# Optimization experiments

Measured on AMD Instinct MI355X. Metric: run time of the kernel, lower is better.

## Reference

```python
import jax, jax.numpy as jnp
import numpy as np

B, T, F, S, H, A = 32768, 64, 64, 5, 128, 16  # batch, obs_len, fut_len, state, hidden, adapter


def _gru_cell(x, h, Wih, Whh, bih, bhh):
    # PyTorch GRUCell math: gates ordered (r, z, n)
    gx = x @ Wih.T + bih
    gh = h @ Whh.T + bhh
    rx, zx, nx = jnp.split(gx, 3, axis=-1)
    rh, zh, nh = jnp.split(gh, 3, axis=-1)
    r = jax.nn.sigmoid(rx + rh)
    z = jax.nn.sigmoid(zx + zh)
    n = jnp.tanh(nx + r * nh)
    return (1.0 - z) * n + z * h


def setup_inputs() -> dict:
    key = jax.random.key(0)
    ks = jax.random.split(key, 24)
    p = lambda k, shp: jax.random.normal(k, shp, jnp.float32) * 0.05
    return {
        "obs": jax.random.normal(ks[0], (B, T, S), jnp.float32),
        "target": jax.random.normal(ks[1], (B, F, S), jnp.float32),
        "dataset_ids": jax.random.randint(ks[2], (B,), 0, 4),
        "enc_Wih": p(ks[3], (3 * H, S)), "enc_Whh": p(ks[4], (3 * H, H)),
        "enc_bih": p(ks[5], (3 * H,)), "enc_bhh": p(ks[6], (3 * H,)),
        "cell_Wih": p(ks[7], (3 * H, S)), "cell_Whh": p(ks[8], (3 * H, H)),
        "cell_bih": p(ks[9], (3 * H,)), "cell_bhh": p(ks[10], (3 * H,)),
        "head_W": p(ks[11], (S, H)), "head_b": p(ks[12], (S,)),
        "pp_W1": p(ks[13], (A, H)), "pp_b1": p(ks[14], (A,)),
        "pp_W2": p(ks[15], (H, A)), "pp_b2": p(ks[16], (H,)),
        "pk_W1": p(ks[17], (A, H)), "pk_b1": p(ks[18], (A,)),
        "pk_W2": p(ks[19], (H, A)), "pk_b2": p(ks[20], (H,)),
    }


def reference(obs, target, dataset_ids,
              enc_Wih, enc_Whh, enc_bih, enc_bhh,
              cell_Wih, cell_Whh, cell_bih, cell_bhh,
              head_W, head_b,
              pp_W1, pp_b1, pp_W2, pp_b2,
              pk_W1, pk_b1, pk_W2, pk_b2):
    b = obs.shape[0]
    # Encoder GRU over obs -> final hidden state [B, H]
    h0 = jnp.zeros((b, H), obs.dtype)
    def enc_step(h, x):
        return _gru_cell(x, h, enc_Wih, enc_Whh, enc_bih, enc_bhh), None
    h_t, _ = jax.lax.scan(enc_step, h0, jnp.swapaxes(obs, 0, 1))

    pm = (dataset_ids == 0)[:, None]  # pointodyssey routed to private_point
    km = (dataset_ids == 1)[:, None]  # kubric routed to private_kubric

    def adapt(h):
        dp = jax.nn.relu(h @ pp_W1.T + pp_b1) @ pp_W2.T + pp_b2
        dk = jax.nn.relu(h @ pk_W1.T + pk_b1) @ pk_W2.T + pk_b2
        return h + jnp.where(pm, dp, 0.0) + jnp.where(km, dk, 0.0)

    # Teacher-forced inputs: x_0 = obs[:, -1], x_t = target[:, t-1]
    xs = jnp.concatenate([obs[:, -1:, :], target[:, :-1, :]], axis=1)  # [B, F, S]
    def roll_step(h, x):
        h = _gru_cell(x, h, cell_Wih, cell_Whh, cell_bih, cell_bhh)
        h = adapt(h)
        return h, h @ head_W.T + head_b
    _, preds = jax.lax.scan(roll_step, h_t, jnp.swapaxes(xs, 0, 1))  # [F, B, S]
    return jnp.swapaxes(preds, 0, 1)  # [B, F, S]
```

## Files before the change

kernel.cpp:

```cpp
#include <hip/hip_runtime.h>

#define B_TOT 32768
#define T_OBS 64
#define F_FUT 64
#define S_DIM 5
#define H_DIM 128
#define A_DIM 16
#define R_BLK 64
#define NTHREADS 512
#define XSTR 320
#define HSTR 128
#define XPAD 36
#define APAD 24

#define LOG2E 1.4426950408889634f
#define L2E2  2.8853900817779268f

typedef __attribute__((ext_vector_type(8))) short short8;
typedef __attribute__((ext_vector_type(4))) float f32x4;

union U8 { short8 v; unsigned int u[4]; unsigned short s[8]; };

#if __has_builtin(__builtin_amdgcn_exp2f)
#define EXP2(x) __builtin_amdgcn_exp2f(x)
#else
#define EXP2(x) exp2f(x)
#endif

__device__ __forceinline__ unsigned short f2bf(float f) {
  unsigned int u = __float_as_uint(f);
  u += 0x7FFFu + ((u >> 16) & 1u);
  return (unsigned short)(u >> 16);
}

__device__ __forceinline__ unsigned cvtpk(float a, float b) {
  unsigned r;
  asm("v_cvt_pk_bf16_f32 %0, %1, %2" : "=v"(r) : "v"(a), "v"(b));
  return r;
}

__device__ __forceinline__ f32x4 MFMA(short8 a, short8 b, f32x4 c) {
  return __builtin_amdgcn_mfma_f32_16x16x32_bf16(a, b, c, 0, 0, 0);
}

__device__ __forceinline__ short8 h_read(const unsigned short* base, int row, int ks, int lg) {
  return *(const short8*)(base + row * HSTR + (((4 * ks + lg + row) & 15) << 3));
}
__device__ __forceinline__ void h_write(unsigned short* base, int row, int w, int lg,
                                        unsigned lo, unsigned hi) {
  unsigned short* p = base + row * HSTR +
                      (((4 * (w >> 1) + lg + row) & 15) << 3) + ((w & 1) << 2);
  *(uint2*)p = make_uint2(lo, hi);
}

__device__ __forceinline__ short8 load_w(const float* __restrict__ W, int ld,
                                         int g0, int gmax, int kmax, int ks,
                                         int lr, int lg, float scale) {
  U8 a;
  const int g = g0 + lr;
  #pragma unroll
  for (int i = 0; i < 8; ++i) {
    int k = 32 * ks + 16 * (i >> 2) + 4 * lg + (i & 3);
    float v = (g < gmax && k < kmax) ? W[g * ld + k] * scale : 0.0f;
    a.s[i] = f2bf(v);
  }
  return a.v;
}

__device__ __forceinline__ void setup_weights(
    const float* __restrict__ Wih, const float* __restrict__ Whh,
    const float* __restrict__ bih, const float* __restrict__ bhh,
    short8 (&fh)[3][4], short8 (&fx)[3],
    f32x4& brz0, f32x4& brz1, f32x4& bnh, f32x4& bnx,
    int w, int lr, int lg)
{
  #pragma unroll
  for (int t = 0; t < 3; ++t) {
    const float sc = (t == 2) ? L2E2 : LOG2E;
    #pragma unroll
    for (int ks = 0; ks < 4; ++ks)
      fh[t][ks] = load_w(Whh, H_DIM, t * H_DIM + 16 * w, 384, H_DIM, ks, lr, lg, sc);
    fx[t] = load_w(Wih, S_DIM, t * H_DIM + 16 * w, 384, S_DIM, 0, lr, lg, sc);
  }
  #pragma unroll
  for (int i = 0; i < 4; ++i) {
    int g = 16 * w + 4 * lg + i;
    brz0[i] = (bih[g] + bhh[g]) * LOG2E;
    brz1[i] = (bih[H_DIM + g] + bhh[H_DIM + g]) * LOG2E;
    bnh[i]  = bhh[2 * H_DIM + g] * L2E2;
    bnx[i]  = bih[2 * H_DIM + g] * L2E2;
  }
}

__device__ __forceinline__ void mfma_rt(
    const unsigned short* __restrict__ hb, const unsigned short* __restrict__ xb,
    int row, int lg,
    const short8 (&fh)[3][4], const short8 (&fx)[3],
    const f32x4& brz0, const f32x4& brz1, const f32x4& bnh, const f32x4& bnx,
    f32x4& aR, f32x4& aZ, f32x4& aN, f32x4& aX)
{
  U8 bx;
  { uint2 t = *(const uint2*)(xb + row * XPAD + 4 * lg);
    bx.u[0] = t.x; bx.u[1] = t.y; bx.u[2] = 0u; bx.u[3] = 0u; }
  short8 bh0 = h_read(hb, row, 0, lg);
  short8 bh1 = h_read(hb, row, 1, lg);
  short8 bh2 = h_read(hb, row, 2, lg);
  short8 bh3 = h_read(hb, row, 3, lg);
  __builtin_amdgcn_s_setprio(1);
  aR = MFMA(fh[0][0], bh0, brz0);
  aR = MFMA(fh[0][1], bh1, aR);
  aR = MFMA(fh[0][2], bh2, aR);
  aR = MFMA(fh[0][3], bh3, aR);
  aR = MFMA(fx[0], bx.v, aR);
  aZ = MFMA(fh[1][0], bh0, brz1);
  aZ = MFMA(fh[1][1], bh1, aZ);
  aZ = MFMA(fh[1][2], bh2, aZ);
  aZ = MFMA(fh[1][3], bh3, aZ);
  aZ = MFMA(fx[1], bx.v, aZ);
  aN = MFMA(fh[2][0], bh0, bnh);
  aN = MFMA(fh[2][1], bh1, aN);
  aN = MFMA(fh[2][2], bh2, aN);
  aN = MFMA(fh[2][3], bh3, aN);
  aX = MFMA(fx[2], bx.v, bnx);
  __builtin_amdgcn_s_setprio(0);
}

__device__ __forceinline__ void act_rt(
    const f32x4& aR, const f32x4& aZ, const f32x4& aN, const f32x4& aX,
    float (&hreg)[4], unsigned short* __restrict__ hd,
    int row, int w, int lg)
{
  float hv[4];
  #pragma unroll
  for (int i = 0; i < 4; ++i) {
    float r = __builtin_amdgcn_rcpf(1.0f + EXP2(-aR[i]));
    float z = __builtin_amdgcn_rcpf(1.0f + EXP2(-aZ[i]));
    float v = fmaf(r, aN[i], aX[i]);
    float q = __builtin_amdgcn_rcpf(1.0f + EXP2(-v));
    float n = fmaf(2.0f, q, -1.0f);
    float h = fmaf(z, hreg[i] - n, n);
    hreg[i] = h; hv[i] = h;
  }
  h_write(hd, row, w, lg, cvtpk(hv[0], hv[1]), cvtpk(hv[2], hv[3]));
}

__device__ __forceinline__ void gru_step(
    const unsigned short* __restrict__ hb, const unsigned short* __restrict__ xb,
    unsigned short* __restrict__ hd,
    const short8 (&fh)[3][4], const short8 (&fx)[3],
    const f32x4& brz0, const f32x4& brz1, const f32x4& bnh, const f32x4& bnx,
    float (&h_reg)[4][4], int w, int lr, int lg)
{
  f32x4 aR0, aZ0, aN0, aX0, aR1, aZ1, aN1, aX1;
  mfma_rt(hb, xb, 0 * 16 + lr, lg, fh, fx, brz0, brz1, bnh, bnx, aR0, aZ0, aN0, aX0);
  mfma_rt(hb, xb, 1 * 16 + lr, lg, fh, fx, brz0, brz1, bnh, bnx, aR1, aZ1, aN1, aX1);
  act_rt(aR0, aZ0, aN0, aX0, h_reg[0], hd, 0 * 16 + lr, w, lg);
  mfma_rt(hb, xb, 2 * 16 + lr, lg, fh, fx, brz0, brz1, bnh, bnx, aR0, aZ0, aN0, aX0);
  act_rt(aR1, aZ1, aN1, aX1, h_reg[1], hd, 1 * 16 + lr, w, lg);
  mfma_rt(hb, xb, 3 * 16 + lr, lg, fh, fx, brz0, brz1, bnh, bnx, aR1, aZ1, aN1, aX1);
  act_rt(aR0, aZ0, aN0, aX0, h_reg[2], hd, 2 * 16 + lr, w, lg);
  act_rt(aR1, aZ1, aN1, aX1, h_reg[3], hd, 3 * 16 + lr, w, lg);
}

__global__ __launch_bounds__(NTHREADS, 2) void trace_gru_kernel(
    const float* __restrict__ obs, const float* __restrict__ target,
    const int* __restrict__ ids,
    const float* __restrict__ eWih, const float* __restrict__ eWhh,
    const float* __restrict__ ebih, const float* __restrict__ ebhh,
    const float* __restrict__ cWih, const float* __restrict__ cWhh,
    const float* __restrict__ cbih, const float* __restrict__ cbhh,
    const float* __restrict__ headW, const float* __restrict__ headb,
    const float* __restrict__ ppW1, const float* __restrict__ ppb1,
    const float* __restrict__ ppW2, const float* __restrict__ ppb2,
    const float* __restrict__ pkW1, const float* __restrict__ pkb1,
    const float* __restrict__ pkW2, const float* __restrict__ pkb2,
    float* __restrict__ out)
{
  __shared__ __align__(16) unsigned short h_lds[2][R_BLK * HSTR];
  __shared__ __align__(16) unsigned short x_lds[2][R_BLK * XPAD];
  __shared__ __align__(16) unsigned short a_lds[2 * R_BLK * APAD];
  __shared__ __align__(16) unsigned short wd_lds[12 * 64 * 8];

  const int tid = threadIdx.x;
  const int lane = tid & 63;
  const int w = tid >> 6;
  const int lr = lane & 15;
  const int lg = lane >> 4;
  const int row0 = blockIdx.x * R_BLK;

  {
    unsigned int* p = (unsigned int*)&h_lds[0][0];
    for (int i = tid; i < R_BLK * HSTR / 2; i += NTHREADS) p[i] = 0u;
    unsigned int* q = (unsigned int*)&x_lds[0][0];
    for (int i = tid; i < 2 * R_BLK * XPAD / 2; i += NTHREADS) q[i] = 0u;
  }

  const bool xa = (tid < R_BLK * S_DIM);
  const int sx_row = tid / 5;
  const int sx_s = tid - 5 * sx_row;
  const float* pobs = obs + (size_t)(row0 + sx_row) * XSTR + sx_s;
  const float* ptgt = target + (size_t)(row0 + sx_row) * XSTR + sx_s;
  float xe = 0.f;

  float pmf[4], kmf[4];
  #pragma unroll
  for (int rt = 0; rt < 4; ++rt) {
    int id = ids[row0 + rt * 16 + lr];
    pmf[rt] = (id == 0) ? 1.0f : 0.0f;
    kmf[rt] = (id == 1) ? 1.0f : 0.0f;
  }

  short8 fh[3][4], fx[3];
  f32x4 brz0, brz1, bnh, bnx;
  setup_weights(eWih, eWhh, ebih, ebhh, fh, fx, brz0, brz1, bnh, bnx, w, lr, lg);

  float h_reg[4][4];
  #pragma unroll
  for (int rt = 0; rt < 4; ++rt)
    #pragma unroll
    for (int i = 0; i < 4; ++i) h_reg[rt][i] = 0.0f;

  __syncthreads();
  if (xa) {
    x_lds[0][sx_row * XPAD + sx_s] = f2bf(pobs[0]);
    xe = pobs[5];
  }
  __syncthreads();

  for (int it = 0; it < T_OBS / 2; ++it) {
    const int u = 2 * it;
    float xn = 0.f;
    if (xa) {
      int v = u + 2;
      xn = (v < 64) ? pobs[v * 5] : pobs[315];
    }
    gru_step(&h_lds[0][0], &x_lds[0][0], &h_lds[1][0],
             fh, fx, brz0, brz1, bnh, bnx, h_reg, w, lr, lg);
    if (xa) x_lds[1][sx_row * XPAD + sx_s] = f2bf(xe);
    __syncthreads();
    xe = xn;
    xn = 0.f;
    if (xa) {
      int v = u + 3;
      xn = (v < 64) ? pobs[v * 5] : ptgt[0];
    }
    gru_step(&h_lds[1][0], &x_lds[1][0], &h_lds[0][0],
             fh, fx, brz0, brz1, bnh, bnx, h_reg, w, lr, lg);
    if (xa) x_lds[0][sx_row * XPAD + sx_s] = f2bf(xe);
    __syncthreads();
    xe = xn;
  }

  setup_weights(cWih, cWhh, cbih, cbhh, fh, fx, brz0, brz1, bnh, bnx, w, lr, lg);
  short8 fW2[2];
  fW2[0] = load_w(ppW2, A_DIM, 16 * w, H_DIM, A_DIM, 0, lr, lg, 1.0f);
  fW2[1] = load_w(pkW2, A_DIM, 16 * w, H_DIM, A_DIM, 0, lr, lg, 1.0f);
  f32x4 b1v, b2v0, b2v1, hbv;
  {
    const float* b1p = (w & 1) ? pkb1 : ppb1;
    #pragma unroll
    for (int i = 0; i < 4; ++i) {
      b1v[i]  = b1p[4 * lg + i];
      b2v0[i] = ppb2[16 * w + 4 * lg + i];
      b2v1[i] = pkb2[16 * w + 4 * lg + i];
      int s = 4 * lg + i;
      hbv[i] = (s < S_DIM) ? headb[s] : 0.0f;
    }
  }
  for (int f = w; f < 12; f += 8) {
    short8 v;
    if (f < 8) {
      const float* W1 = (f >> 2) ? pkW1 : ppW1;
      v = load_w(W1, H_DIM, 0, A_DIM, H_DIM, f & 3, lr, lg, 1.0f);
    } else {
      v = load_w(headW, H_DIM, 0, S_DIM, H_DIM, f - 8, lr, lg, 1.0f);
    }
    *(short8*)&wd_lds[(f * 64 + lane) * 8] = v;
  }
  __syncthreads();

  for (int d = 0; d < F_FUT; ++d) {
    float xn = 0.f;
    if (xa) xn = (d < 63) ? ptgt[(d + 1) * 5] : ptgt[315];
    gru_step(&h_lds[0][0], &x_lds[d & 1][0], &h_lds[1][0],
             fh, fx, brz0, brz1, bnh, bnx, h_reg, w, lr, lg);
    __syncthreads();

    {
      const int aa = w & 1;
      const int arow = (w >> 1) * 16 + lr;
      short8 b0 = h_read(&h_lds[1][0], arow, 0, lg);
      f32x4 acc = MFMA(*(const short8*)&wd_lds[((aa * 4 + 0) * 64 + lane) * 8], b0, b1v);
      #pragma unroll
      for (int ks = 1; ks < 4; ++ks) {
        short8 bh = h_read(&h_lds[1][0], arow, ks, lg);
        acc = MFMA(*(const short8*)&wd_lds[((aa * 4 + ks) * 64 + lane) * 8], bh, acc);
      }
      unsigned lo = cvtpk(fmaxf(acc[0], 0.f), fmaxf(acc[1], 0.f));
      unsigned hi = cvtpk(fmaxf(acc[2], 0.f), fmaxf(acc[3], 0.f));
      *(uint2*)&a_lds[(aa * R_BLK + arow) * APAD + 4 * lg] = make_uint2(lo, hi);
    }
    __syncthreads();

    #pragma unroll
    for (int rt = 0; rt < 4; ++rt) {
      const int arow = rt * 16 + lr;
      U8 a0, a1;
      { uint2 t = *(const uint2*)&a_lds[(0 * R_BLK + arow) * APAD + 4 * lg];
        a0.u[0] = t.x; a0.u[1] = t.y; a0.u[2] = 0u; a0.u[3] = 0u; }
      { uint2 t = *(const uint2*)&a_lds[(1 * R_BLK + arow) * APAD + 4 * lg];
        a1.u[0] = t.x; a1.u[1] = t.y; a1.u[2] = 0u; a1.u[3] = 0u; }
      f32x4 d0 = MFMA(fW2[0], a0.v, b2v0);
      f32x4 d1 = MFMA(fW2[1], a1.v, b2v1);
      float hv[4];
      #pragma unroll
      for (int i = 0; i < 4; ++i) {
        float h = h_reg[rt][i] + pmf[rt] * d0[i] + kmf[rt] * d1[i];
        h_reg[rt][i] = h; hv[i] = h;
      }
      h_write(&h_lds[0][0], arow, w, lg, cvtpk(hv[0], hv[1]), cvtpk(hv[2], hv[3]));
    }
    if (xa && d < 63) x_lds[(d + 1) & 1][sx_row * XPAD + sx_s] = f2bf(xe);
    __syncthreads();

    if (w < 4) {
      const int arow = w * 16 + lr;
      short8 b0 = h_read(&h_lds[0][0], arow, 0, lg);
      f32x4 acc = MFMA(*(const short8*)&wd_lds[((8 + 0) * 64 + lane) * 8], b0, hbv);
      #pragma unroll
      for (int ks = 1; ks < 4; ++ks) {
        short8 bh = h_read(&h_lds[0][0], arow, ks, lg);
        acc = MFMA(*(const short8*)&wd_lds[((8 + ks) * 64 + lane) * 8], bh, acc);
      }
      float* op = out + (size_t)((row0 + arow) * F_FUT + d) * S_DIM;
      if (lg == 0) { op[0] = acc[0]; op[1] = acc[1]; op[2] = acc[2]; op[3] = acc[3]; }
      else if (lg == 1) { op[4] = acc[0]; }
    }
    xe = xn;
  }
}

extern "C" void kernel_launch(void* const* d_in, const int* in_sizes, int n_in,
                              void* d_out, int out_size, void* d_ws, size_t ws_size,
                              hipStream_t stream) {
  (void)in_sizes; (void)n_in; (void)out_size; (void)d_ws; (void)ws_size;
  const float* obs    = (const float*)d_in[0];
  const float* target = (const float*)d_in[1];
  const int*   ids    = (const int*)d_in[2];
  const float* eWih = (const float*)d_in[3];
  const float* eWhh = (const float*)d_in[4];
  const float* ebih = (const float*)d_in[5];
  const float* ebhh = (const float*)d_in[6];
  const float* cWih = (const float*)d_in[7];
  const float* cWhh = (const float*)d_in[8];
  const float* cbih = (const float*)d_in[9];
  const float* cbhh = (const float*)d_in[10];
  const float* headW = (const float*)d_in[11];
  const float* headb = (const float*)d_in[12];
  const float* ppW1 = (const float*)d_in[13];
  const float* ppb1 = (const float*)d_in[14];
  const float* ppW2 = (const float*)d_in[15];
  const float* ppb2 = (const float*)d_in[16];
  const float* pkW1 = (const float*)d_in[17];
  const float* pkb1 = (const float*)d_in[18];
  const float* pkW2 = (const float*)d_in[19];
  const float* pkb2 = (const float*)d_in[20];

  dim3 grid(B_TOT / R_BLK), block(NTHREADS);
  trace_gru_kernel<<<grid, block, 0, stream>>>(
      obs, target, ids,
      eWih, eWhh, ebih, ebhh,
      cWih, cWhh, cbih, cbhh,
      headW, headb,
      ppW1, ppb1, ppW2, ppb2,
      pkW1, pkb1, pkW2, pkb2,
      (float*)d_out);
}
```

Before: 656.0 us.

## Compute adapter down-projection redundantly per wave to drop LDS staging and barrier

Each wave now computes both adapters' first-layer activations for all four row tiles itself, instead of splitting that work across waves and sharing it through an LDS buffer. This removes the a_lds scratch buffer, its writes and reads, and one __syncthreads per decode step. In exchange each wave does eight times the first-layer MFMA work (32 instead of 4 MFMAs per step) and reads more of h_lds.

```diff
diff --git a/kernel.cpp b/kernel.cpp
--- a/kernel.cpp
+++ b/kernel.cpp
@@ -11,7 +11,6 @@
 #define XSTR 320
 #define HSTR 128
 #define XPAD 36
-#define APAD 24
 
 #define LOG2E 1.4426950408889634f
 #define L2E2  2.8853900817779268f
@@ -178,7 +177,6 @@
 {
   __shared__ __align__(16) unsigned short h_lds[2][R_BLK * HSTR];
   __shared__ __align__(16) unsigned short x_lds[2][R_BLK * XPAD];
-  __shared__ __align__(16) unsigned short a_lds[2 * R_BLK * APAD];
   __shared__ __align__(16) unsigned short wd_lds[12 * 64 * 8];
 
   const int tid = threadIdx.x;
@@ -255,17 +253,15 @@
   short8 fW2[2];
   fW2[0] = load_w(ppW2, A_DIM, 16 * w, H_DIM, A_DIM, 0, lr, lg, 1.0f);
   fW2[1] = load_w(pkW2, A_DIM, 16 * w, H_DIM, A_DIM, 0, lr, lg, 1.0f);
-  f32x4 b1v, b2v0, b2v1, hbv;
-  {
-    const float* b1p = (w & 1) ? pkb1 : ppb1;
-    #pragma unroll
-    for (int i = 0; i < 4; ++i) {
-      b1v[i]  = b1p[4 * lg + i];
-      b2v0[i] = ppb2[16 * w + 4 * lg + i];
-      b2v1[i] = pkb2[16 * w + 4 * lg + i];
-      int s = 4 * lg + i;
-      hbv[i] = (s < S_DIM) ? headb[s] : 0.0f;
-    }
+  f32x4 b1v0, b1v1, b2v0, b2v1, hbv;
+  #pragma unroll
+  for (int i = 0; i < 4; ++i) {
+    b1v0[i] = ppb1[4 * lg + i];
+    b1v1[i] = pkb1[4 * lg + i];
+    b2v0[i] = ppb2[16 * w + 4 * lg + i];
+    b2v1[i] = pkb2[16 * w + 4 * lg + i];
+    int s = 4 * lg + i;
+    hbv[i] = (s < S_DIM) ? headb[s] : 0.0f;
   }
   for (int f = w; f < 12; f += 8) {
     short8 v;
@@ -286,32 +282,30 @@
              fh, fx, brz0, brz1, bnh, bnx, h_reg, w, lr, lg);
     __syncthreads();
 
-    {
-      const int aa = w & 1;
-      const int arow = (w >> 1) * 16 + lr;
-      short8 b0 = h_read(&h_lds[1][0], arow, 0, lg);
-      f32x4 acc = MFMA(*(const short8*)&wd_lds[((aa * 4 + 0) * 64 + lane) * 8], b0, b1v);
-      #pragma unroll
-      for (int ks = 1; ks < 4; ++ks) {
-        short8 bh = h_read(&h_lds[1][0], arow, ks, lg);
-        acc = MFMA(*(const short8*)&wd_lds[((aa * 4 + ks) * 64 + lane) * 8], bh, acc);
-      }
-      unsigned lo = cvtpk(fmaxf(acc[0], 0.f), fmaxf(acc[1], 0.f));
-      unsigned hi = cvtpk(fmaxf(acc[2], 0.f), fmaxf(acc[3], 0.f));
-      *(uint2*)&a_lds[(aa * R_BLK + arow) * APAD + 4 * lg] = make_uint2(lo, hi);
-    }
-    __syncthreads();
-
     #pragma unroll
     for (int rt = 0; rt < 4; ++rt) {
       const int arow = rt * 16 + lr;
-      U8 a0, a1;
-      { uint2 t = *(const uint2*)&a_lds[(0 * R_BLK + arow) * APAD + 4 * lg];
-        a0.u[0] = t.x; a0.u[1] = t.y; a0.u[2] = 0u; a0.u[3] = 0u; }
-      { uint2 t = *(const uint2*)&a_lds[(1 * R_BLK + arow) * APAD + 4 * lg];
-        a1.u[0] = t.x; a1.u[1] = t.y; a1.u[2] = 0u; a1.u[3] = 0u; }
-      f32x4 d0 = MFMA(fW2[0], a0.v, b2v0);
-      f32x4 d1 = MFMA(fW2[1], a1.v, b2v1);
+      short8 bh0 = h_read(&h_lds[1][0], arow, 0, lg);
+      short8 bh1 = h_read(&h_lds[1][0], arow, 1, lg);
+      short8 bh2 = h_read(&h_lds[1][0], arow, 2, lg);
+      short8 bh3 = h_read(&h_lds[1][0], arow, 3, lg);
+      f32x4 accP = MFMA(*(const short8*)&wd_lds[(0 * 64 + lane) * 8], bh0, b1v0);
+      accP = MFMA(*(const short8*)&wd_lds[(1 * 64 + lane) * 8], bh1, accP);
+      accP = MFMA(*(const short8*)&wd_lds[(2 * 64 + lane) * 8], bh2, accP);
+      accP = MFMA(*(const short8*)&wd_lds[(3 * 64 + lane) * 8], bh3, accP);
+      f32x4 accK = MFMA(*(const short8*)&wd_lds[(4 * 64 + lane) * 8], bh0, b1v1);
+      accK = MFMA(*(const short8*)&wd_lds[(5 * 64 + lane) * 8], bh1, accK);
+      accK = MFMA(*(const short8*)&wd_lds[(6 * 64 + lane) * 8], bh2, accK);
+      accK = MFMA(*(const short8*)&wd_lds[(7 * 64 + lane) * 8], bh3, accK);
+      U8 pa, ka;
+      pa.u[0] = cvtpk(fmaxf(accP[0], 0.f), fmaxf(accP[1], 0.f));
+      pa.u[1] = cvtpk(fmaxf(accP[2], 0.f), fmaxf(accP[3], 0.f));
+      pa.u[2] = 0u; pa.u[3] = 0u;
+      ka.u[0] = cvtpk(fmaxf(accK[0], 0.f), fmaxf(accK[1], 0.f));
+      ka.u[1] = cvtpk(fmaxf(accK[2], 0.f), fmaxf(accK[3], 0.f));
+      ka.u[2] = 0u; ka.u[3] = 0u;
+      f32x4 d0 = MFMA(fW2[0], pa.v, b2v0);
+      f32x4 d1 = MFMA(fW2[1], ka.v, b2v1);
       float hv[4];
       #pragma unroll
       for (int i = 0; i < 4; ++i) {
```

New measurement: 731.2 us. +11.5%, slower.
